# Kernel optimization log

Hardware: AMD Instinct MI355X
Metric: run time of the kernel (lower is better)

## Reference

```python
import jax, jax.numpy as jnp
import numpy as np

EPS = 1e-4  # self.epsilon

@jax.custom_vjp
def heavi_tanh(x):
    # forward: hard heaviside H(x) = 0 for x<=0 else 1
    return jnp.where(x <= 0.0, 0.0, 1.0).astype(x.dtype)

def _heavi_fwd(x):
    return heavi_tanh(x), x

def _heavi_bwd(x, dy):
    # surrogate gradient: d/dx [0.5 + 0.5*tanh(k*x)] with k=1 -> 1 - tanh(x)^2
    return (dy * (1.0 - jnp.tanh(x) ** 2),)

heavi_tanh.defvjp(_heavi_fwd, _heavi_bwd)

def setup_inputs() -> dict:
    key = jax.random.key(0)
    k1, k2, k3 = jax.random.split(key, 3)
    B, D = 2048, 3706
    return {
        "fake_tensor": jax.random.uniform(k1, (B, D), dtype=jnp.float32),
        "min_boundary_value": jax.random.uniform(k2, (D,), dtype=jnp.float32),
        "interval_lengths": jax.random.uniform(k3, (D, 4), dtype=jnp.float32),
    }

def reference(fake_tensor, min_boundary_value, interval_lengths):
    # boundary values: b[:,0]=min_boundary, b[:,i]=b[:,i-1]+relu(len[:,i-1])+eps  -> cumsum
    steps = jax.nn.relu(interval_lengths) + EPS                      # [D,4]
    b = jnp.cumsum(jnp.concatenate([min_boundary_value[:, None], steps], axis=1), axis=1)  # [D,5]

    r = jnp.arange(6.0, dtype=fake_tensor.dtype)                     # target ratings 0..5
    k = jnp.arange(5.0, dtype=fake_tensor.dtype)                     # boundary idx 0..4
    s = jnp.sign(r[:, None] - k[None, :] - 0.5)                      # [6,5] constant sign matrix

    p2 = fake_tensor[:, :, None] - b[None, :, :]                     # [B,D,5] a - b_jk
    x = s[None, None, :, :] * p2[:, :, None, :]                      # [B,D,6,5]
    dist = jnp.prod(heavi_tanh(x), axis=-1)                          # [B,D,6]
    val = dist @ r                                                   # [B,D]
    return dist, val
```

## Files before the change

### kernel.cpp

```cpp
#include <hip/hip_runtime.h>

#define EPS 1e-4f

constexpr int B = 2048;
constexpr int D = 3706;
constexpr int NP = B * D / 2;
constexpr int BLK = 256;

__device__ __forceinline__ void bucketize(float a, float mb, float4 L,
                                          float* __restrict__ r6, float& v) {
    const float s0 = fmaxf(L.x, 0.0f) + EPS;
    const float s1 = fmaxf(L.y, 0.0f) + EPS;
    const float s2 = fmaxf(L.z, 0.0f) + EPS;
    const float s3 = fmaxf(L.w, 0.0f) + EPS;
    const float b0 = mb;
    const float b1 = b0 + s0;
    const float b2 = b1 + s1;
    const float b3 = b2 + s2;
    const float b4 = b3 + s3;

    const int cnt = (int)(a > b0) + (int)(a > b1) + (int)(a > b2)
                  + (int)(a > b3) + (int)(a > b4);
    const bool eq = (a == b0) | (a == b1) | (a == b2) | (a == b3) | (a == b4);
    const float ok = eq ? 0.0f : 1.0f;

#pragma unroll
    for (int r = 0; r < 6; ++r) r6[r] = (r == cnt) ? ok : 0.0f;
    v = eq ? 0.0f : (float)cnt;
}

__global__ __launch_bounds__(256) void disc_kernel(
        const float* __restrict__ fake,
        const float* __restrict__ minb,
        const float* __restrict__ lens,
        float* __restrict__ out) {
    __shared__ float4 sd[3 * BLK];

    const int t = threadIdx.x;
    const int p = blockIdx.x * BLK + t;
    const int flat = p << 1;
    const int d0 = flat % D;

    const float2 a2 = reinterpret_cast<const float2*>(fake)[p];
    const float2 mb = *reinterpret_cast<const float2*>(minb + d0);
    const float4 L0 = reinterpret_cast<const float4*>(lens)[d0];
    const float4 L1 = reinterpret_cast<const float4*>(lens)[d0 + 1];

    float r0[6], r1[6], v0, v1;
    bucketize(a2.x, mb.x, L0, r0, v0);
    bucketize(a2.y, mb.y, L1, r1, v1);

    sd[t * 3 + 0] = make_float4(r0[0], r0[1], r0[2], r0[3]);
    sd[t * 3 + 1] = make_float4(r0[4], r0[5], r1[0], r1[1]);
    sd[t * 3 + 2] = make_float4(r1[2], r1[3], r1[4], r1[5]);

    float* val = out + (size_t)B * D * 6;
    reinterpret_cast<float2*>(val)[p] = make_float2(v0, v1);

    __syncthreads();

    float4* dp = reinterpret_cast<float4*>(out) + (size_t)blockIdx.x * (3 * BLK);
    dp[t]           = sd[t];
    dp[t + BLK]     = sd[t + BLK];
    dp[t + 2 * BLK] = sd[t + 2 * BLK];
}

extern "C" void kernel_launch(void* const* d_in, const int* in_sizes, int n_in,
                              void* d_out, int out_size, void* d_ws, size_t ws_size,
                              hipStream_t stream) {
    const float* fake = (const float*)d_in[0];
    const float* minb = (const float*)d_in[1];
    const float* lens = (const float*)d_in[2];
    float* out = (float*)d_out;

    const int grid = NP / BLK;
    disc_kernel<<<grid, BLK, 0, stream>>>(fake, minb, lens, out);
}
```

Before: 238.4 us.

## Use persistent grid-stride blocks with prefetched loads and double-buffered LDS staging

Replaces the one-tile-per-block launch with a fixed grid of 1536 persistent blocks that loop over tiles. Each iteration prefetches the next tile's inputs while the current one is computed, and alternates between two shared-memory buffers so only one barrier is needed per tile. The LDS layout also changes to a strided order that should reduce bank conflicts on writes. The aim is to hide load latency and cut block launch overhead in a write-bandwidth-bound kernel, at the cost of more registers and less parallelism from the smaller grid.

Measured after the change: 247.4 us. +3.8%, slower.

```diff
diff --git a/kernel.cpp b/kernel.cpp
--- a/kernel.cpp
+++ b/kernel.cpp
@@ -2,12 +2,18 @@
 
 #define EPS 1e-4f
 
+typedef float v2f __attribute__((ext_vector_type(2)));
+typedef float v4f __attribute__((ext_vector_type(4)));
+
 constexpr int B = 2048;
 constexpr int D = 3706;
-constexpr int NP = B * D / 2;
+constexpr int NE = B * D;
+constexpr int NP = NE / 2;
 constexpr int BLK = 256;
+constexpr int NTILES = NP / BLK;
+constexpr int GRIDB = 1536;
 
-__device__ __forceinline__ void bucketize(float a, float mb, float4 L,
+__device__ __forceinline__ void bucketize(float a, float mb, v4f L,
                                           float* __restrict__ r6, float& v) {
     const float s0 = fmaxf(L.x, 0.0f) + EPS;
     const float s1 = fmaxf(L.y, 0.0f) + EPS;
@@ -34,35 +40,58 @@
         const float* __restrict__ minb,
         const float* __restrict__ lens,
         float* __restrict__ out) {
-    __shared__ float4 sd[3 * BLK];
+    __shared__ v4f sd[2][3 * BLK];
 
     const int t = threadIdx.x;
-    const int p = blockIdx.x * BLK + t;
-    const int flat = p << 1;
-    const int d0 = flat % D;
+    float* valbase = out + (size_t)NE * 6;
 
-    const float2 a2 = reinterpret_cast<const float2*>(fake)[p];
-    const float2 mb = *reinterpret_cast<const float2*>(minb + d0);
-    const float4 L0 = reinterpret_cast<const float4*>(lens)[d0];
-    const float4 L1 = reinterpret_cast<const float4*>(lens)[d0 + 1];
+    auto ldtile = [&](int tile, v2f& a, v2f& mb, v4f& L0, v4f& L1) {
+        const int p = tile * BLK + t;
+        const unsigned d0 = ((unsigned)p * 2u) % (unsigned)D;
+        a  = reinterpret_cast<const v2f*>(fake)[p];
+        mb = *reinterpret_cast<const v2f*>(minb + d0);
+        L0 = reinterpret_cast<const v4f*>(lens)[d0];
+        L1 = reinterpret_cast<const v4f*>(lens)[d0 + 1];
+    };
 
-    float r0[6], r1[6], v0, v1;
-    bucketize(a2.x, mb.x, L0, r0, v0);
-    bucketize(a2.y, mb.y, L1, r1, v1);
+    int tile = blockIdx.x;
+    v2f a, mb; v4f L0, L1;
+    ldtile(tile, a, mb, L0, L1);
+    int h = 0;
 
-    sd[t * 3 + 0] = make_float4(r0[0], r0[1], r0[2], r0[3]);
-    sd[t * 3 + 1] = make_float4(r0[4], r0[5], r1[0], r1[1]);
-    sd[t * 3 + 2] = make_float4(r1[2], r1[3], r1[4], r1[5]);
+    while (true) {
+        const int ntile = tile + GRIDB;
+        const bool has_next = ntile < NTILES;
+        v2f an, mbn; v4f L0n, L1n;
+        if (has_next) ldtile(ntile, an, mbn, L0n, L1n);
 
-    float* val = out + (size_t)B * D * 6;
-    reinterpret_cast<float2*>(val)[p] = make_float2(v0, v1);
+        float r0[6], r1[6], v0, v1;
+        bucketize(a.x, mb.x, L0, r0, v0);
+        bucketize(a.y, mb.y, L1, r1, v1);
 
-    __syncthreads();
+        reinterpret_cast<v2f*>(valbase)[tile * BLK + t] = (v2f){v0, v1};
 
-    float4* dp = reinterpret_cast<float4*>(out) + (size_t)blockIdx.x * (3 * BLK);
-    dp[t]           = sd[t];
-    dp[t + BLK]     = sd[t + BLK];
-    dp[t + 2 * BLK] = sd[t + 2 * BLK];
+        v4f* sh = sd[h];
+        sh[0 * BLK + t] = (v4f){r0[0], r0[1], r0[2], r0[3]};
+        sh[1 * BLK + t] = (v4f){r0[4], r0[5], r1[0], r1[1]};
+        sh[2 * BLK + t] = (v4f){r1[2], r1[3], r1[4], r1[5]};
+
+        __syncthreads();
+
+        v4f* dp = reinterpret_cast<v4f*>(out) + (size_t)tile * (3 * BLK);
+#pragma unroll
+        for (int m = 0; m < 3; ++m) {
+            const int j = m * BLK + t;
+            const int src = j / 3;
+            const int k = j - src * 3;
+            dp[j] = sh[k * BLK + src];
+        }
+
+        if (!has_next) break;
+        tile = ntile;
+        h ^= 1;
+        a = an; mb = mbn; L0 = L0n; L1 = L1n;
+    }
 }
 
 extern "C" void kernel_launch(void* const* d_in, const int* in_sizes, int n_in,
@@ -73,6 +102,5 @@
     const float* lens = (const float*)d_in[2];
     float* out = (float*)d_out;
 
-    const int grid = NP / BLK;
-    disc_kernel<<<grid, BLK, 0, stream>>>(fake, minb, lens, out);
+    disc_kernel<<<GRIDB, BLK, 0, stream>>>(fake, minb, lens, out);
 }
```
